# Kernel tuning notes

Measured on AMD Instinct MI355X. Metric: run time of the kernel, lower is better.

The kernel has to match this reference:

```python
import jax, jax.numpy as jnp
import numpy as np

N_HEAD = 16


def setup_inputs() -> dict:
    key = jax.random.key(0)
    ks = jax.random.split(key, 9)
    B, T, C = 4, 2048, 1024
    s = 1.0 / np.sqrt(C)
    x = jax.random.normal(ks[0], (B, T, C), dtype=jnp.float32)
    Wq = jax.random.normal(ks[1], (C, C), dtype=jnp.float32) * s
    bq = jax.random.normal(ks[2], (C,), dtype=jnp.float32) * 0.01
    Wk = jax.random.normal(ks[3], (C, C), dtype=jnp.float32) * s
    bk = jax.random.normal(ks[4], (C,), dtype=jnp.float32) * 0.01
    Wv = jax.random.normal(ks[5], (C, C), dtype=jnp.float32) * s
    bv = jax.random.normal(ks[6], (C,), dtype=jnp.float32) * 0.01
    Wp = jax.random.normal(ks[7], (C, C), dtype=jnp.float32) * s
    bp = jax.random.normal(ks[8], (C,), dtype=jnp.float32) * 0.01
    return {"x": x, "Wq": Wq, "bq": bq, "Wk": Wk, "bk": bk,
            "Wv": Wv, "bv": bv, "Wp": Wp, "bp": bp}


def reference(x, Wq, bq, Wk, bk, Wv, bv, Wp, bp):
    B, T, C = x.shape
    H = N_HEAD
    d = C // H
    # projections (torch Linear: x @ W.T + b)
    q = (x @ Wq.T + bq).reshape(B, T, H, d)  # [B,T,H,d]
    k = (x @ Wk.T + bk).reshape(B, T, H, d)
    v = (x @ Wv.T + bv).reshape(B, T, H, d)
    scale = 1.0 / jnp.sqrt(jnp.asarray(d, dtype=x.dtype))
    # scores: [B,H,T,T]
    att = jnp.einsum('bqhd,bkhd->bhqk', q, k) * scale
    causal = jnp.tril(jnp.ones((T, T), dtype=bool))  # [T,T]
    att = jnp.where(causal[None, None], att, jnp.asarray(-jnp.inf, dtype=att.dtype))
    att = jax.nn.softmax(att, axis=-1)
    y = jnp.einsum('bhqk,bkhd->bqhd', att, v).reshape(B, T, C)
    return y @ Wp.T + bp
```

## Files before the change

### kernel.cpp

```cpp
#include <hip/hip_runtime.h>
#include <hip/hip_bf16.h>

typedef __attribute__((ext_vector_type(8))) short bf16x8;
typedef __attribute__((ext_vector_type(4))) float f32x4;

static constexpr int Tt = 2048;
static constexpr int Cc = 1024;
static constexpr int Dd = 64;
static constexpr int Mm = 8192;

static constexpr size_t XN = (size_t)Mm * Cc;
static constexpr size_t WN = (size_t)Cc * Cc;

__device__ __forceinline__ void async_copy16(void* lds, const void* g) {
  __builtin_amdgcn_global_load_lds(
      (const __attribute__((address_space(1))) void*)g,
      (__attribute__((address_space(3))) void*)lds, 16, 0, 0);
}

__device__ __forceinline__ unsigned short f2bf(float f) {
  union { float f; unsigned int u; } v; v.f = f;
  unsigned int r = (v.u + 0x7fffu + ((v.u >> 16) & 1u)) >> 16;
  return (unsigned short)r;
}
__device__ __forceinline__ unsigned int pack2bf(float f0, float f1) {
  unsigned int b0 = __float_as_uint(f0) + 0x8000u;
  unsigned int b1 = __float_as_uint(f1) + 0x8000u;
  return (b1 & 0xffff0000u) | (b0 >> 16);
}
__device__ __forceinline__ unsigned int cvtpk2bf(float f0, float f1) {
  unsigned int r;
  asm("v_cvt_pk_bf16_f32 %0, %1, %2" : "=v"(r) : "v"(f0), "v"(f1));
  return r;
}
__device__ __forceinline__ uint4 ldconv_f32(const float* p) {
  float4 lo = *(const float4*)p;
  float4 hi = *(const float4*)(p + 4);
  uint4 r;
  r.x = pack2bf(lo.x, lo.y);
  r.y = pack2bf(lo.z, lo.w);
  r.z = pack2bf(hi.x, hi.y);
  r.w = pack2bf(hi.z, hi.w);
  return r;
}

__global__ __launch_bounds__(256) void convert_all(
    const float* __restrict__ x, const float* __restrict__ wq,
    const float* __restrict__ wk, const float* __restrict__ wv,
    unsigned short* __restrict__ dst)
{
  const size_t i = ((size_t)blockIdx.x * 256 + threadIdx.x) * 8;
  const float* s; size_t off;
  if (i < XN)                { s = x;  off = 0; }
  else if (i < XN + WN)      { s = wq; off = XN; }
  else if (i < XN + 2 * WN)  { s = wk; off = XN + WN; }
  else                       { s = wv; off = XN + 2 * WN; }
  *(uint4*)(dst + i) = ldconv_f32(s + (i - off));
}

template <int MODE>
__device__ __forceinline__ void gemm_async_body(
    unsigned short* As, unsigned short* Bs,
    const unsigned short* __restrict__ A,
    const unsigned short* __restrict__ Bt,
    const float* __restrict__ bias,
    unsigned short* __restrict__ out, float mult)
{
  const int tid  = threadIdx.x;
  const int wave = tid >> 6;
  const int lane = tid & 63;
  const int m16  = lane & 15;
  const int quad = lane >> 4;
  const int row0 = blockIdx.x * 128;
  const int col0 = blockIdx.y * 128;
  const int wm = (wave >> 1) * 64;
  const int wn = (wave & 1) * 64;

  f32x4 acc[4][4] = {};

  const int c0 = tid, c1 = 256 + tid;
  const unsigned short* Ag0 = A  + (size_t)(row0 + (c0 >> 2)) * Cc + (c0 & 3) * 8;
  const unsigned short* Ag1 = A  + (size_t)(row0 + (c1 >> 2)) * Cc + (c1 & 3) * 8;
  const unsigned short* Bg0 = Bt + (size_t)(col0 + (c0 >> 2)) * Cc + (c0 & 3) * 8;
  const unsigned short* Bg1 = Bt + (size_t)(col0 + (c1 >> 2)) * Cc + (c1 & 3) * 8;
  char* Al0 = (char*)As + wave * 1024;
  char* Al1 = (char*)As + 4096 + wave * 1024;
  char* Bl0 = (char*)Bs + wave * 1024;
  char* Bl1 = (char*)Bs + 4096 + wave * 1024;

  for (int k0 = 0; k0 < Cc; k0 += 32) {
    __syncthreads();
    async_copy16(Al0, Ag0 + k0);
    async_copy16(Al1, Ag1 + k0);
    async_copy16(Bl0, Bg0 + k0);
    async_copy16(Bl1, Bg1 + k0);
    __syncthreads();
    bf16x8 af[4], bfr[4];
#pragma unroll
    for (int i = 0; i < 4; ++i)
      af[i] = *(const bf16x8*)(As + (wm + i * 16 + m16) * 32 + quad * 8);
#pragma unroll
    for (int j = 0; j < 4; ++j)
      bfr[j] = *(const bf16x8*)(Bs + (wn + j * 16 + m16) * 32 + quad * 8);
#pragma unroll
    for (int i = 0; i < 4; ++i)
#pragma unroll
      for (int j = 0; j < 4; ++j)
        acc[i][j] = __builtin_amdgcn_mfma_f32_16x16x32_bf16(af[i], bfr[j], acc[i][j], 0, 0, 0);
  }

#pragma unroll
  for (int i = 0; i < 4; ++i) {
    const int rbase = row0 + wm + i * 16 + quad * 4;
#pragma unroll
    for (int j = 0; j < 4; ++j) {
      const int col = col0 + wn + j * 16 + m16;
      const float bv = bias[col];
      if (MODE == 0) {
#pragma unroll
        for (int r = 0; r < 4; ++r)
          out[(size_t)(rbase + r) * Cc + col] = f2bf((acc[i][j][r] + bv) * mult);
      } else {
        const int t0 = rbase & (Tt - 1);
        const int b  = rbase >> 11;
        ushort4 pk;
        pk.x = f2bf(acc[i][j][0] + bv);
        pk.y = f2bf(acc[i][j][1] + bv);
        pk.z = f2bf(acc[i][j][2] + bv);
        pk.w = f2bf(acc[i][j][3] + bv);
        *(ushort4*)(out + (size_t)(b * Cc + col) * Tt + t0) = pk;
      }
    }
  }
}

__global__ __launch_bounds__(256) void qkv_gemm(
    const unsigned short* __restrict__ Xb,
    const unsigned short* __restrict__ Wqb, const float* __restrict__ bq,
    const unsigned short* __restrict__ Wkb, const float* __restrict__ bk,
    const unsigned short* __restrict__ Wvb, const float* __restrict__ bv,
    unsigned short* Qw, unsigned short* Kw, unsigned short* Vtw)
{
  __shared__ __align__(16) unsigned short smem[8192];
  const int z = blockIdx.z;
  if (z == 0)      gemm_async_body<0>(smem, smem + 4096, Xb, Wqb, bq, Qw, 0.125f * 1.44269504f);
  else if (z == 1) gemm_async_body<0>(smem, smem + 4096, Xb, Wkb, bk, Kw, 1.0f);
  else             gemm_async_body<1>(smem, smem + 4096, Xb, Wvb, bv, Vtw, 1.0f);
}

__global__ __launch_bounds__(256) void attn_pair(
    const unsigned short* __restrict__ Q,
    const unsigned short* __restrict__ Kg,
    const unsigned short* __restrict__ Vt,
    unsigned short* __restrict__ Y)
{
  __shared__ __align__(16) unsigned short KV[2 * 8192];

  const int tid  = threadIdx.x;
  const int wave = tid >> 6;
  const int lane = tid & 63;
  const int m16  = lane & 15;
  const int quad = lane >> 4;

  const int p  = blockIdx.x;
  const int bh = blockIdx.y;
  const int b = bh >> 4, h = bh & 15;

  const unsigned short* Kb = Kg + (size_t)(b * Tt) * Cc + h * Dd;
  const unsigned short* Vb = Vt + (size_t)(b * Cc + h * Dd) * Tt;

  const int maxH = 32 - 2 * p;
  const int TOT  = 34;
  const int chp  = quad ^ ((m16 >> 1) & 3);

  bf16x8 onesA;
#pragma unroll
  for (int i = 0; i < 8; ++i) onesA[i] = (short)0x3F80;

  int kkS[2], rrS[2], chdS[2];
#pragma unroll
  for (int ii = 0; ii < 2; ++ii) {
    const int cc = ii * 256 + tid;
    kkS[ii]  = cc >> 8;
    rrS[ii]  = (cc >> 2) & 63;
    chdS[ii] = (cc & 3) ^ ((rrS[ii] >> 1) & 3);
  }

  int sidx = 63 - 4 * p - wave;
  int qw = sidx * 32;
  int nk = (sidx >> 1) + 1;
  bf16x8 qf[2][2];
  {
    const unsigned short* Qb = Q + (size_t)(b * Tt + qw) * Cc + h * Dd;
#pragma unroll
    for (int s = 0; s < 2; ++s)
#pragma unroll
      for (int kk = 0; kk < 2; ++kk)
        qf[s][kk] = *(const bf16x8*)(Qb + (size_t)(s * 16 + m16) * Cc + kk * 32 + quad * 8);
  }
  f32x4 o[2][4] = {};
  f32x4 lz[2] = {};

  auto writeout = [&](int qw_) {
#pragma unroll
    for (int s = 0; s < 2; ++s) {
      const float l = lz[s][0];
      const float inv = (l > 0.f) ? (1.0f / l) : 0.f;
      const int t = qw_ + s * 16 + m16;
      unsigned short* yp = Y + (size_t)(b * Tt + t) * Cc + h * Dd + quad * 4;
#pragma unroll
      for (int jn = 0; jn < 4; ++jn) {
        uint2 pk;
        pk.x = cvtpk2bf(o[s][jn][0] * inv, o[s][jn][1] * inv);
        pk.y = cvtpk2bf(o[s][jn][2] * inv, o[s][jn][3] * inv);
        *(uint2*)(yp + jn * 16) = pk;
      }
    }
  };

  {
    char* KbufB = (char*)KV;
    char* VbufB = KbufB + 8192;
#pragma unroll
    for (int ii = 0; ii < 2; ++ii) {
      async_copy16(KbufB + ii * 4096 + wave * 1024,
                   Kb + (size_t)rrS[ii] * Cc + kkS[ii] * 32 + chdS[ii] * 8);
      async_copy16(VbufB + ii * 4096 + wave * 1024,
                   Vb + (size_t)rrS[ii] * Tt + kkS[ii] * 32 + chdS[ii] * 8);
    }
  }

  for (int g = 0; g < TOT; ++g) {
    if (g == maxH) {
      writeout(qw);
      sidx = 4 * p + wave;
      qw = sidx * 32;
      nk = (sidx >> 1) + 1;
      const unsigned short* Qb = Q + (size_t)(b * Tt + qw) * Cc + h * Dd;
#pragma unroll
      for (int s = 0; s < 2; ++s) {
#pragma unroll
        for (int kk = 0; kk < 2; ++kk)
          qf[s][kk] = *(const bf16x8*)(Qb + (size_t)(s * 16 + m16) * Cc + kk * 32 + quad * 8);
#pragma unroll
        for (int jn = 0; jn < 4; ++jn)
          o[s][jn] = f32x4{0.f, 0.f, 0.f, 0.f};
        lz[s] = f32x4{0.f, 0.f, 0.f, 0.f};
      }
    }
    const int kt  = (g < maxH) ? g : g - maxH;
    const int k0  = kt * 64;
    const int buf = g & 1;

    __syncthreads();
    if (g + 1 < TOT) {
      const int g1  = g + 1;
      const int kt1 = (g1 < maxH) ? g1 : g1 - maxH;
      const int k1  = kt1 * 64;
      char* KbufB = (char*)KV + (buf ^ 1) * 16384;
      char* VbufB = KbufB + 8192;
#pragma unroll
      for (int ii = 0; ii < 2; ++ii) {
        async_copy16(KbufB + ii * 4096 + wave * 1024,
                     Kb + (size_t)(k1 + rrS[ii]) * Cc + kkS[ii] * 32 + chdS[ii] * 8);
        async_copy16(VbufB + ii * 4096 + wave * 1024,
                     Vb + (size_t)rrS[ii] * Tt + k1 + kkS[ii] * 32 + chdS[ii] * 8);
      }
    }

    if (kt < nk) {
      const unsigned short* Kbuf = KV + buf * 8192;
      const unsigned short* Vbuf = Kbuf + 4096;
      bf16x8 kf[2][4], vf[2][4];
#pragma unroll
      for (int kk = 0; kk < 2; ++kk)
#pragma unroll
        for (int jn = 0; jn < 4; ++jn) {
          kf[kk][jn] = *(const bf16x8*)(Kbuf + kk * 2048 + (jn * 16 + m16) * 32 + chp * 8);
          vf[kk][jn] = *(const bf16x8*)(Vbuf + kk * 2048 + (jn * 16 + m16) * 32 + chp * 8);
        }

#pragma unroll
      for (int s = 0; s < 2; ++s) {
        const int smin = qw + s * 16;
        if (k0 > smin + 15) continue;
        f32x4 sv[4] = {};
        __builtin_amdgcn_s_setprio(1);
#pragma unroll
        for (int kk = 0; kk < 2; ++kk)
#pragma unroll
          for (int jn = 0; jn < 4; ++jn)
            sv[jn] = __builtin_amdgcn_mfma_f32_16x16x32_bf16(kf[kk][jn], qf[s][kk], sv[jn], 0, 0, 0);
        __builtin_amdgcn_s_setprio(0);

        if (k0 + 63 <= smin) {
#pragma unroll
          for (int jn = 0; jn < 4; ++jn)
#pragma unroll
            for (int r = 0; r < 4; ++r)
              sv[jn][r] = __builtin_exp2f(sv[jn][r]);
        } else {
          const int qcol = smin + m16;
#pragma unroll
          for (int jn = 0; jn < 4; ++jn)
#pragma unroll
            for (int r = 0; r < 4; ++r)
              sv[jn][r] = (k0 + jn * 16 + quad * 4 + r > qcol)
                              ? 0.f : __builtin_exp2f(sv[jn][r]);
        }

        unsigned int P2[4][2];
#pragma unroll
        for (int jn = 0; jn < 4; ++jn) {
          P2[jn][0] = cvtpk2bf(sv[jn][0], sv[jn][1]);
          P2[jn][1] = cvtpk2bf(sv[jn][2], sv[jn][3]);
        }
#pragma unroll
        for (int kk = 0; kk < 2; ++kk) {
          auto r0 = __builtin_amdgcn_permlane32_swap(P2[2 * kk][0], P2[2 * kk + 1][0], false, false);
          auto t0 = __builtin_amdgcn_permlane16_swap(r0[0], r0[1], false, false);
          auto r1 = __builtin_amdgcn_permlane32_swap(P2[2 * kk][1], P2[2 * kk + 1][1], false, false);
          auto t1 = __builtin_amdgcn_permlane16_swap(r1[0], r1[1], false, false);
          uint4 u;
          u.x = t0[0];
          u.y = t1[0];
          u.z = t0[1];
          u.w = t1[1];
          union { uint4 u4; bf16x8 bf; } cv; cv.u4 = u;
          __builtin_amdgcn_s_setprio(1);
          lz[s] = __builtin_amdgcn_mfma_f32_16x16x32_bf16(onesA, cv.bf, lz[s], 0, 0, 0);
#pragma unroll
          for (int jn = 0; jn < 4; ++jn)
            o[s][jn] = __builtin_amdgcn_mfma_f32_16x16x32_bf16(vf[kk][jn], cv.bf, o[s][jn], 0, 0, 0);
          __builtin_amdgcn_s_setprio(0);
        }
      }
    }
  }

  writeout(qw);
}

__global__ __launch_bounds__(256) void proj_gemm(
    const unsigned short* __restrict__ Y,
    const float* __restrict__ Wp, const float* __restrict__ bp,
    float* __restrict__ out)
{
  __shared__ __align__(16) unsigned short As[4096];
  __shared__ __align__(16) unsigned short Bs[4096];
  const int tid  = threadIdx.x;
  const int wave = tid >> 6;
  const int lane = tid & 63;
  const int m16  = lane & 15;
  const int quad = lane >> 4;
  const int row0 = blockIdx.x * 128;
  const int col0 = blockIdx.y * 128;
  const int wm = (wave >> 1) * 64;
  const int wn = (wave & 1) * 64;

  f32x4 acc[4][4] = {};

  const int c0 = tid, c1 = 256 + tid;
  const unsigned short* Ag0 = Y + (size_t)(row0 + (c0 >> 2)) * Cc + (c0 & 3) * 8;
  const unsigned short* Ag1 = Y + (size_t)(row0 + (c1 >> 2)) * Cc + (c1 & 3) * 8;
  const float* Bg0 = Wp + (size_t)(col0 + (c0 >> 2)) * Cc + (c0 & 3) * 8;
  const float* Bg1 = Wp + (size_t)(col0 + (c1 >> 2)) * Cc + (c1 & 3) * 8;
  char* Al0 = (char*)As + wave * 1024;
  char* Al1 = (char*)As + 4096 + wave * 1024;

  uint4 b0 = ldconv_f32(Bg0);
  uint4 b1 = ldconv_f32(Bg1);

  for (int k0 = 0; k0 < Cc; k0 += 32) {
    __syncthreads();
    async_copy16(Al0, Ag0 + k0);
    async_copy16(Al1, Ag1 + k0);
    *(uint4*)(Bs + (size_t)c0 * 8) = b0;
    *(uint4*)(Bs + (size_t)c1 * 8) = b1;
    __syncthreads();
    if (k0 + 32 < Cc) {
      b0 = ldconv_f32(Bg0 + k0 + 32);
      b1 = ldconv_f32(Bg1 + k0 + 32);
    }
    bf16x8 af[4], bfr[4];
#pragma unroll
    for (int i = 0; i < 4; ++i)
      af[i] = *(const bf16x8*)(As + (wm + i * 16 + m16) * 32 + quad * 8);
#pragma unroll
    for (int j = 0; j < 4; ++j)
      bfr[j] = *(const bf16x8*)(Bs + (wn + j * 16 + m16) * 32 + quad * 8);
#pragma unroll
    for (int i = 0; i < 4; ++i)
#pragma unroll
      for (int j = 0; j < 4; ++j)
        acc[i][j] = __builtin_amdgcn_mfma_f32_16x16x32_bf16(af[i], bfr[j], acc[i][j], 0, 0, 0);
  }

#pragma unroll
  for (int i = 0; i < 4; ++i) {
    const int rbase = row0 + wm + i * 16 + quad * 4;
#pragma unroll
    for (int j = 0; j < 4; ++j) {
      const int col = col0 + wn + j * 16 + m16;
      const float bv = bp[col];
#pragma unroll
      for (int r = 0; r < 4; ++r)
        out[(size_t)(rbase + r) * Cc + col] = acc[i][j][r] + bv;
    }
  }
}

extern "C" void kernel_launch(void* const* d_in, const int* in_sizes, int n_in,
                              void* d_out, int out_size, void* d_ws, size_t ws_size,
                              hipStream_t stream)
{
  const float* x  = (const float*)d_in[0];
  const float* Wq = (const float*)d_in[1];
  const float* bq = (const float*)d_in[2];
  const float* Wk = (const float*)d_in[3];
  const float* bk = (const float*)d_in[4];
  const float* Wv = (const float*)d_in[5];
  const float* bv = (const float*)d_in[6];
  const float* Wp = (const float*)d_in[7];
  const float* bp = (const float*)d_in[8];

  unsigned short* ws  = (unsigned short*)d_ws;
  unsigned short* Qw  = ws;
  unsigned short* Kw  = ws + (size_t)1 * XN;
  unsigned short* Vtw = ws + (size_t)2 * XN;
  unsigned short* Yw  = ws + (size_t)3 * XN;

  unsigned short* cvt = (unsigned short*)d_out;
  unsigned short* Xb  = cvt;
  unsigned short* Wqb = cvt + XN;
  unsigned short* Wkb = cvt + XN + WN;
  unsigned short* Wvb = cvt + XN + 2 * WN;
  float* out = (float*)d_out;

  convert_all<<<5632, 256, 0, stream>>>(x, Wq, Wk, Wv, cvt);
  qkv_gemm<<<dim3(64, 8, 3), 256, 0, stream>>>(Xb, Wqb, bq, Wkb, bk, Wvb, bv, Qw, Kw, Vtw);
  attn_pair<<<dim3(8, 64), 256, 0, stream>>>(Qw, Kw, Vtw, Yw);
  proj_gemm<<<dim3(64, 8), 256, 0, stream>>>(Yw, Wp, bp, out);
}
```

Baseline: 294.3 us.

## Double-buffer LDS tiles and XOR-swizzle layout in QKV and projection GEMMs

```diff
diff --git a/kernel.cpp b/kernel.cpp
--- a/kernel.cpp
+++ b/kernel.cpp
@@ -75,38 +75,49 @@
   const int col0 = blockIdx.y * 128;
   const int wm = (wave >> 1) * 64;
   const int wn = (wave & 1) * 64;
+  const int chp = quad ^ ((m16 >> 1) & 3);
 
   f32x4 acc[4][4] = {};
 
   const int c0 = tid, c1 = 256 + tid;
-  const unsigned short* Ag0 = A  + (size_t)(row0 + (c0 >> 2)) * Cc + (c0 & 3) * 8;
-  const unsigned short* Ag1 = A  + (size_t)(row0 + (c1 >> 2)) * Cc + (c1 & 3) * 8;
-  const unsigned short* Bg0 = Bt + (size_t)(col0 + (c0 >> 2)) * Cc + (c0 & 3) * 8;
-  const unsigned short* Bg1 = Bt + (size_t)(col0 + (c1 >> 2)) * Cc + (c1 & 3) * 8;
-  char* Al0 = (char*)As + wave * 1024;
-  char* Al1 = (char*)As + 4096 + wave * 1024;
-  char* Bl0 = (char*)Bs + wave * 1024;
-  char* Bl1 = (char*)Bs + 4096 + wave * 1024;
-
+  const int sw0 = (c0 & 3) ^ ((c0 >> 3) & 3);
+  const int sw1 = (c1 & 3) ^ ((c1 >> 3) & 3);
+  const unsigned short* Ag0 = A  + (size_t)(row0 + (c0 >> 2)) * Cc + sw0 * 8;
+  const unsigned short* Ag1 = A  + (size_t)(row0 + (c1 >> 2)) * Cc + sw1 * 8;
+  const unsigned short* Bg0 = Bt + (size_t)(col0 + (c0 >> 2)) * Cc + sw0 * 8;
+  const unsigned short* Bg1 = Bt + (size_t)(col0 + (c1 >> 2)) * Cc + sw1 * 8;
+
+  async_copy16((char*)As + wave * 1024,        Ag0);
+  async_copy16((char*)As + 4096 + wave * 1024, Ag1);
+  async_copy16((char*)Bs + wave * 1024,        Bg0);
+  async_copy16((char*)Bs + 4096 + wave * 1024, Bg1);
+
+  int buf = 0;
   for (int k0 = 0; k0 < Cc; k0 += 32) {
     __syncthreads();
-    async_copy16(Al0, Ag0 + k0);
-    async_copy16(Al1, Ag1 + k0);
-    async_copy16(Bl0, Bg0 + k0);
-    async_copy16(Bl1, Bg1 + k0);
-    __syncthreads();
+    if (k0 + 32 < Cc) {
+      char* Ab = (char*)As + (buf ^ 1) * 8192;
+      char* Bb = (char*)Bs + (buf ^ 1) * 8192;
+      async_copy16(Ab + wave * 1024,        Ag0 + k0 + 32);
+      async_copy16(Ab + 4096 + wave * 1024, Ag1 + k0 + 32);
+      async_copy16(Bb + wave * 1024,        Bg0 + k0 + 32);
+      async_copy16(Bb + 4096 + wave * 1024, Bg1 + k0 + 32);
+    }
+    const unsigned short* Asb = As + buf * 4096;
+    const unsigned short* Bsb = Bs + buf * 4096;
     bf16x8 af[4], bfr[4];
 #pragma unroll
     for (int i = 0; i < 4; ++i)
-      af[i] = *(const bf16x8*)(As + (wm + i * 16 + m16) * 32 + quad * 8);
+      af[i] = *(const bf16x8*)(Asb + (wm + i * 16 + m16) * 32 + chp * 8);
 #pragma unroll
     for (int j = 0; j < 4; ++j)
-      bfr[j] = *(const bf16x8*)(Bs + (wn + j * 16 + m16) * 32 + quad * 8);
+      bfr[j] = *(const bf16x8*)(Bsb + (wn + j * 16 + m16) * 32 + chp * 8);
 #pragma unroll
     for (int i = 0; i < 4; ++i)
 #pragma unroll
       for (int j = 0; j < 4; ++j)
         acc[i][j] = __builtin_amdgcn_mfma_f32_16x16x32_bf16(af[i], bfr[j], acc[i][j], 0, 0, 0);
+    buf ^= 1;
   }
 
 #pragma unroll
@@ -141,11 +152,11 @@
     const unsigned short* __restrict__ Wvb, const float* __restrict__ bv,
     unsigned short* Qw, unsigned short* Kw, unsigned short* Vtw)
 {
-  __shared__ __align__(16) unsigned short smem[8192];
+  __shared__ __align__(16) unsigned short smem[16384];
   const int z = blockIdx.z;
-  if (z == 0)      gemm_async_body<0>(smem, smem + 4096, Xb, Wqb, bq, Qw, 0.125f * 1.44269504f);
-  else if (z == 1) gemm_async_body<0>(smem, smem + 4096, Xb, Wkb, bk, Kw, 1.0f);
-  else             gemm_async_body<1>(smem, smem + 4096, Xb, Wvb, bv, Vtw, 1.0f);
+  if (z == 0)      gemm_async_body<0>(smem, smem + 8192, Xb, Wqb, bq, Qw, 0.125f * 1.44269504f);
+  else if (z == 1) gemm_async_body<0>(smem, smem + 8192, Xb, Wkb, bk, Kw, 1.0f);
+  else             gemm_async_body<1>(smem, smem + 8192, Xb, Wvb, bv, Vtw, 1.0f);
 }
 
 __global__ __launch_bounds__(256) void attn_pair(
@@ -346,8 +357,8 @@
     const float* __restrict__ Wp, const float* __restrict__ bp,
     float* __restrict__ out)
 {
-  __shared__ __align__(16) unsigned short As[4096];
-  __shared__ __align__(16) unsigned short Bs[4096];
+  __shared__ __align__(16) unsigned short As[8192];
+  __shared__ __align__(16) unsigned short Bs[8192];
   const int tid  = threadIdx.x;
   const int wave = tid >> 6;
   const int lane = tid & 63;
@@ -357,43 +368,59 @@
   const int col0 = blockIdx.y * 128;
   const int wm = (wave >> 1) * 64;
   const int wn = (wave & 1) * 64;
+  const int chp = quad ^ ((m16 >> 1) & 3);
 
   f32x4 acc[4][4] = {};
 
   const int c0 = tid, c1 = 256 + tid;
-  const unsigned short* Ag0 = Y + (size_t)(row0 + (c0 >> 2)) * Cc + (c0 & 3) * 8;
-  const unsigned short* Ag1 = Y + (size_t)(row0 + (c1 >> 2)) * Cc + (c1 & 3) * 8;
+  const int sw0 = (c0 & 3) ^ ((c0 >> 3) & 3);
+  const int sw1 = (c1 & 3) ^ ((c1 >> 3) & 3);
+  const unsigned short* Ag0 = Y + (size_t)(row0 + (c0 >> 2)) * Cc + sw0 * 8;
+  const unsigned short* Ag1 = Y + (size_t)(row0 + (c1 >> 2)) * Cc + sw1 * 8;
   const float* Bg0 = Wp + (size_t)(col0 + (c0 >> 2)) * Cc + (c0 & 3) * 8;
   const float* Bg1 = Wp + (size_t)(col0 + (c1 >> 2)) * Cc + (c1 & 3) * 8;
-  char* Al0 = (char*)As + wave * 1024;
-  char* Al1 = (char*)As + 4096 + wave * 1024;
+  const int bd0 = ((c0 >> 2) * 4 + sw0) * 8;
+  const int bd1 = ((c1 >> 2) * 4 + sw1) * 8;
 
   uint4 b0 = ldconv_f32(Bg0);
   uint4 b1 = ldconv_f32(Bg1);
 
+  async_copy16((char*)As + wave * 1024,        Ag0);
+  async_copy16((char*)As + 4096 + wave * 1024, Ag1);
+  *(uint4*)(Bs + bd0) = b0;
+  *(uint4*)(Bs + bd1) = b1;
+  b0 = ldconv_f32(Bg0 + 32);
+  b1 = ldconv_f32(Bg1 + 32);
+
+  int buf = 0;
   for (int k0 = 0; k0 < Cc; k0 += 32) {
     __syncthreads();
-    async_copy16(Al0, Ag0 + k0);
-    async_copy16(Al1, Ag1 + k0);
-    *(uint4*)(Bs + (size_t)c0 * 8) = b0;
-    *(uint4*)(Bs + (size_t)c1 * 8) = b1;
-    __syncthreads();
     if (k0 + 32 < Cc) {
-      b0 = ldconv_f32(Bg0 + k0 + 32);
-      b1 = ldconv_f32(Bg1 + k0 + 32);
-    }
+      char* Ab = (char*)As + (buf ^ 1) * 8192;
+      async_copy16(Ab + wave * 1024,        Ag0 + k0 + 32);
+      async_copy16(Ab + 4096 + wave * 1024, Ag1 + k0 + 32);
+      *(uint4*)(Bs + (buf ^ 1) * 4096 + bd0) = b0;
+      *(uint4*)(Bs + (buf ^ 1) * 4096 + bd1) = b1;
+      if (k0 + 64 < Cc) {
+        b0 = ldconv_f32(Bg0 + k0 + 64);
+        b1 = ldconv_f32(Bg1 + k0 + 64);
+      }
+    }
+    const unsigned short* Asb = As + buf * 4096;
+    const unsigned short* Bsb = Bs + buf * 4096;
     bf16x8 af[4], bfr[4];
 #pragma unroll
     for (int i = 0; i < 4; ++i)
-      af[i] = *(const bf16x8*)(As + (wm + i * 16 + m16) * 32 + quad * 8);
+      af[i] = *(const bf16x8*)(Asb + (wm + i * 16 + m16) * 32 + chp * 8);
 #pragma unroll
     for (int j = 0; j < 4; ++j)
-      bfr[j] = *(const bf16x8*)(Bs + (wn + j * 16 + m16) * 32 + quad * 8);
+      bfr[j] = *(const bf16x8*)(Bsb + (wn + j * 16 + m16) * 32 + chp * 8);
 #pragma unroll
     for (int i = 0; i < 4; ++i)
 #pragma unroll
       for (int j = 0; j < 4; ++j)
         acc[i][j] = __builtin_amdgcn_mfma_f32_16x16x32_bf16(af[i], bfr[j], acc[i][j], 0, 0, 0);
+    buf ^= 1;
   }
 
 #pragma unroll
```

Measured after the change: 273.4 us. 7.1% less time.
